# Performance work log

Hardware: AMD Instinct MI355X
Metric: run time of the kernel (lower is better)

The kernel has to match this reference:

```python
import jax, jax.numpy as jnp
import numpy as np


def _diag_gather(x):
    # out[b,c,h,w] = x[b,c,h,(h+w)%W]; then transpose last two dims and flatten
    B, C, H, W = x.shape
    idx = (jnp.arange(H)[:, None] + jnp.arange(W)[None, :]) % W
    g = jnp.take_along_axis(x, idx[None, None], axis=3)  # [B,C,H,W]
    return g.transpose(0, 1, 3, 2).reshape(B, C, H * W)


def _antidiag_gather(x):
    B, C, H, W = x.shape
    idx = (jnp.arange(W)[None, :] - jnp.arange(H)[:, None]) % W
    g = jnp.take_along_axis(x, idx[None, None], axis=3)
    return g.transpose(0, 1, 3, 2).reshape(B, C, H * W)


def _diag_scatter(flat, shape):
    # exact inverse of _diag_gather (per-row circular-shift permutation)
    B, C, H, W = shape
    t = flat.reshape(B, C, W, H).transpose(0, 1, 3, 2)  # [B,C,H,W]
    inv = (jnp.arange(W)[None, :] - jnp.arange(H)[:, None]) % W
    return jnp.take_along_axis(t, inv[None, None], axis=3)


def _antidiag_scatter(flat, shape):
    B, C, H, W = shape
    t = flat.reshape(B, C, W, H).transpose(0, 1, 3, 2)
    inv = (jnp.arange(W)[None, :] + jnp.arange(H)[:, None]) % W
    return jnp.take_along_axis(t, inv[None, None], axis=3)


def cross_scan(x):
    # x: [B,C,H,W] -> xs: [B,8,C,L]; 8 scan directions (row, col, flips, diag, antidiag, flips)
    B, C, H, W = x.shape
    L = H * W
    xf = x.reshape(B, C, L)
    xt = x.transpose(0, 1, 3, 2).reshape(B, C, L)
    xd = _diag_gather(x)
    xa = _antidiag_gather(x)
    return jnp.stack(
        [xf, xt, xf[..., ::-1], xt[..., ::-1], xd, xa, xd[..., ::-1], xa[..., ::-1]],
        axis=1,
    )


def cross_merge(ys):
    # ys: [B,8,D,H,W] -> y: [B,D,L]
    B, K, D, H, W = ys.shape
    L = H * W
    ys = ys.reshape(B, K, D, L)
    a = ys[:, 0:2] + ys[:, 2:4][..., ::-1]
    y = a[:, 0] + a[:, 1].reshape(B, D, W, H).transpose(0, 1, 3, 2).reshape(B, D, L)
    b = ys[:, 4:6] + ys[:, 6:8][..., ::-1]
    y = y + _diag_scatter(b[:, 0], (B, D, H, W)).reshape(B, D, L)
    y = y + _antidiag_scatter(b[:, 1], (B, D, H, W)).reshape(B, D, L)
    return y


def selective_scan(u, delta, A, Bs, Cs, Ds):
    # u, delta: [B,KD,L]; A: [KD,N]; Bs, Cs: [B,K,N,L]; Ds: [KD]
    Bn, KD, L = u.shape
    K = Bs.shape[1]
    Dd = KD // K
    N = A.shape[1]
    dA = jnp.exp(delta[:, :, None, :] * A[None, :, :, None])  # [B,KD,N,L]
    Bexp = jnp.broadcast_to(Bs[:, :, None], (Bn, K, Dd, N, L)).reshape(Bn, KD, N, L)
    Cexp = jnp.broadcast_to(Cs[:, :, None], (Bn, K, Dd, N, L)).reshape(Bn, KD, N, L)
    dBu = delta[:, :, None, :] * Bexp * u[:, :, None, :]

    def comb(c1, c2):
        a1, b1 = c1
        a2, b2 = c2
        return a2 * a1, a2 * b1 + b2

    _, h = jax.lax.associative_scan(comb, (dA, dBu), axis=-1)  # h: [B,KD,N,L]
    return jnp.sum(Cexp * h, axis=2) + Ds[None, :, None] * u


def setup_inputs() -> dict:
    key = jax.random.key(0)
    ks = jax.random.split(key, 8)
    B, D, H, W = 1, 96, 64, 64
    K, N, R = 8, 16, 6
    return {
        "x": jax.random.normal(ks[0], (B, D, H, W), jnp.float32),
        "x_proj_weight": jax.random.normal(ks[1], (K, R + 2 * N, D), jnp.float32) * 0.05,
        "dt_projs_weight": jax.random.normal(ks[2], (K, D, R), jnp.float32) * 0.1,
        "dt_projs_bias": jax.random.normal(ks[3], (K, D), jnp.float32) * 0.1,
        "A_logs": jax.random.uniform(ks[4], (K * D, N), jnp.float32),
        "Ds": jax.random.normal(ks[5], (K * D,), jnp.float32),
        "out_norm_weight": jnp.ones((D,), jnp.float32),
        "out_norm_bias": jnp.zeros((D,), jnp.float32),
    }


def reference(x, x_proj_weight, dt_projs_weight, dt_projs_bias, A_logs, Ds,
              out_norm_weight, out_norm_bias):
    B, D, H, W = x.shape
    K, _, R = dt_projs_weight.shape
    N = A_logs.shape[1]
    L = H * W

    xs = cross_scan(x)  # [B,K,D,L]
    x_dbl = jnp.einsum("bkdl,kcd->bkcl", xs, x_proj_weight)  # [B,K,R+2N,L]
    dts, Bs, Cs = jnp.split(x_dbl, [R, R + N], axis=2)
    dts = jnp.einsum("bkrl,kdr->bkdl", dts, dt_projs_weight)  # [B,K,D,L]

    u = xs.reshape(B, K * D, L)
    delta = jax.nn.softplus(dts.reshape(B, K * D, L)
                            + dt_projs_bias.reshape(-1)[None, :, None])
    A = -jnp.exp(A_logs)  # [KD,N]

    ys = selective_scan(u, delta, A, Bs, Cs, Ds)  # [B,KD,L]
    y = cross_merge(ys.reshape(B, K, D, H, W))  # [B,D,L]

    # out_norm (v0): LayerNorm over channel dim
    y = y.transpose(0, 2, 1)  # [B,L,D]
    mu = jnp.mean(y, axis=-1, keepdims=True)
    var = jnp.var(y, axis=-1, keepdims=True)
    y = (y - mu) * jax.lax.rsqrt(var + 1e-5) * out_norm_weight + out_norm_bias
    return y.reshape(B, H, W, D)
```

## Files before the change

kernel.cpp:

```cpp
#include <hip/hip_runtime.h>
#include <math.h>

#define D_ 96
#define L_ 4096
#define K_ 8
#define N_ 16
#define R_ 6
#define CDBL 38
#define DL_ (D_ * L_)

#define REPN(M) M(0) M(1) M(2) M(3) M(4) M(5) M(6) M(7) \
                M(8) M(9) M(10) M(11) M(12) M(13) M(14) M(15)
#define REP8(M) M(0) M(1) M(2) M(3) M(4) M(5) M(6) M(7)
#define FENCE asm volatile("" ::: "memory");

#if __has_builtin(__builtin_amdgcn_exp2f)
#define EXP2(x) __builtin_amdgcn_exp2f(x)
#else
#define EXP2(x) exp2f(x)
#endif
#if __has_builtin(__builtin_amdgcn_logf)
#define LOG2F(x) __builtin_amdgcn_logf(x)
#else
#define LOG2F(x) __log2f(x)
#endif

#define LOG2E 1.44269504088896340736f
#define LN2F  0.69314718055994530942f

__device__ __forceinline__ int src_index(int k, int l) {
    int h = l & 63, w = l >> 6;
    int lp = 4095 - l;
    int hp = lp & 63, wp = lp >> 6;
    switch (k) {
    case 0: return l;
    case 1: return (h << 6) + w;
    case 2: return lp;
    case 3: return (hp << 6) + wp;
    case 4: return (h << 6) + ((h + w) & 63);
    case 5: return (h << 6) + ((w - h) & 63);
    case 6: return (hp << 6) + ((hp + wp) & 63);
    default: return (hp << 6) + ((wp - hp) & 63);
    }
}

__device__ __forceinline__ int merge_src(int k, int l) {
    int h = l >> 6, w = l & 63;
    int i1 = (w << 6) + h;
    int i4 = (((w - h) & 63) << 6) + h;
    int i5 = (((w + h) & 63) << 6) + h;
    switch (k) {
    case 0: return l;
    case 1: return i1;
    case 2: return 4095 - l;
    case 3: return 4095 - i1;
    case 4: return i4;
    case 5: return i5;
    case 6: return 4095 - i4;
    default: return 4095 - i5;
    }
}

#define PQ(p) ((((p) >> 6) * 66) + ((p) & 63))

__global__ __launch_bounds__(512) void k_xscan(const float* __restrict__ x,
                                               float* __restrict__ xs) {
    __shared__ float img[64 * 66];
    int d = blockIdx.x;
    int t = threadIdx.x;
    const float* xd = x + d * L_;
    #pragma unroll
    for (int i = 0; i < 8; ++i) {
        int l = i * 512 + t;
        img[PQ(l)] = xd[l];
    }
    __syncthreads();
    #pragma unroll
    for (int k = 0; k < K_; ++k) {
        float* dst = xs + (k * D_ + d) * L_;
        #pragma unroll
        for (int i = 0; i < 8; ++i) {
            int l = i * 512 + t;
            dst[l] = img[PQ(src_index(k, l))];
        }
    }
}

__global__ __launch_bounds__(256) void k_xdbl(const float* __restrict__ xs,
                                              const float* __restrict__ wproj,
                                              float* __restrict__ xdbl) {
    __shared__ float tile[64][100];
    int bid = blockIdx.x;
    int swz = (bid & 7) * 64 + (bid >> 3);
    int k = swz >> 6;
    int l0 = (swz & 63) * 64;

    const float* src = xs + k * DL_ + l0;
    for (int e = threadIdx.x; e < D_ * 64; e += 256) {
        int d = e >> 6, li = e & 63;
        tile[li][d] = src[d * L_ + li];
    }
    __syncthreads();

    int lt = threadIdx.x & 63;
    int cg = __builtin_amdgcn_readfirstlane(threadIdx.x >> 6);
    const float* wk = wproj + k * CDBL * D_;
    float acc[10];
    #pragma unroll
    for (int j = 0; j < 10; ++j) acc[j] = 0.f;
    for (int d4 = 0; d4 < D_; d4 += 4) {
        float4 tv = *(const float4*)&tile[lt][d4];
        #pragma unroll
        for (int j = 0; j < 10; ++j) {
            int c = cg + 4 * j;
            if (c < CDBL) {
                float4 wv = *(const float4*)&wk[c * D_ + d4];
                acc[j] = fmaf(tv.x, wv.x, acc[j]);
                acc[j] = fmaf(tv.y, wv.y, acc[j]);
                acc[j] = fmaf(tv.z, wv.z, acc[j]);
                acc[j] = fmaf(tv.w, wv.w, acc[j]);
            }
        }
    }
    #pragma unroll
    for (int j = 0; j < 10; ++j) {
        int c = cg + 4 * j;
        if (c < CDBL) xdbl[(k * CDBL + c) * L_ + l0 + lt] = acc[j];
    }
}


#if __has_builtin(__builtin_amdgcn_update_dpp)
#define HAVE_DPP 1
template<int CTRL, int RM>
__device__ __forceinline__ float updpp(float oldv, float src) {
    int r = __builtin_amdgcn_update_dpp(__builtin_bit_cast(int, oldv),
                                        __builtin_bit_cast(int, src),
                                        CTRL, RM, 0xF, false);
    return __builtin_bit_cast(float, r);
}
#else
#define HAVE_DPP 0
#endif

__global__ __launch_bounds__(512, 3) void k_scan(const float* __restrict__ xdbl,
                                                 const float* __restrict__ dtw,
                                                 const float* __restrict__ dtb,
                                                 const float* __restrict__ alogs,
                                                 const float* __restrict__ dsv_,
                                                 const float* __restrict__ xs,
                                                 float* __restrict__ ys) {
    int bid = blockIdx.x;
    int k = bid & 7;
    int d = bid >> 3;
    int kd = k * D_ + d;
    int t = threadIdx.x;
    int lane = t & 63, wv = t >> 6;
    int l0t = t * 8;

    __shared__ float An_s[16];
    __shared__ float agg_a[8][16], agg_b[8][16];
    __shared__ float cb_s[8][16];
    if (t < 16)
        An_s[t] = -expf(alogs[kd * N_ + t]);

#define DECL(n) float sA##n, sB##n;
    REPN(DECL)
#undef DECL
#define DECL(i) float d##i, u##i, y##i;
    REP8(DECL)
#undef DECL

    const float* xr = xdbl + k * CDBL * L_;
    const float2* wp2 = (const float2*)(dtw + kd * R_);
    const float2 w01 = wp2[0], w23 = wp2[1], w45 = wp2[2];
    const float bias = dtb[kd];
    const float dval = dsv_[kd];
#define SPL2(dst, s) { float p = (s) * LOG2E; \
    float l2 = LOG2F(1.f + EXP2(p)); \
    dst = ((s) > 20.f) ? p : l2; }
#define DLTQ(j, i0, i1, i2, i3) { \
    const float4 r0 = *(const float4*)(xr + 0 * L_ + l0t + j * 4); \
    const float4 r1 = *(const float4*)(xr + 1 * L_ + l0t + j * 4); \
    const float4 r2 = *(const float4*)(xr + 2 * L_ + l0t + j * 4); \
    const float4 r3 = *(const float4*)(xr + 3 * L_ + l0t + j * 4); \
    const float4 r4 = *(const float4*)(xr + 4 * L_ + l0t + j * 4); \
    const float4 r5 = *(const float4*)(xr + 5 * L_ + l0t + j * 4); \
    float s; \
    s = fmaf(w01.x, r0.x, bias); s = fmaf(w01.y, r1.x, s); s = fmaf(w23.x, r2.x, s); \
    s = fmaf(w23.y, r3.x, s); s = fmaf(w45.x, r4.x, s); s = fmaf(w45.y, r5.x, s); \
    SPL2(d##i0, s) \
    s = fmaf(w01.x, r0.y, bias); s = fmaf(w01.y, r1.y, s); s = fmaf(w23.x, r2.y, s); \
    s = fmaf(w23.y, r3.y, s); s = fmaf(w45.x, r4.y, s); s = fmaf(w45.y, r5.y, s); \
    SPL2(d##i1, s) \
    s = fmaf(w01.x, r0.z, bias); s = fmaf(w01.y, r1.z, s); s = fmaf(w23.x, r2.z, s); \
    s = fmaf(w23.y, r3.z, s); s = fmaf(w45.x, r4.z, s); s = fmaf(w45.y, r5.z, s); \
    SPL2(d##i2, s) \
    s = fmaf(w01.x, r0.w, bias); s = fmaf(w01.y, r1.w, s); s = fmaf(w23.x, r2.w, s); \
    s = fmaf(w23.y, r3.w, s); s = fmaf(w45.x, r4.w, s); s = fmaf(w45.y, r5.w, s); \
    SPL2(d##i3, s) }
    DLTQ(0, 0, 1, 2, 3)
    DLTQ(1, 4, 5, 6, 7)
#undef DLTQ
#undef SPL2

    {
        const float* up = xs + kd * L_ + l0t;
        const float4 ua = *(const float4*)(up);
        const float4 ub = *(const float4*)(up + 4);
        u0 = ua.x; u1 = ua.y; u2 = ua.z; u3 = ua.w;
        u4 = ub.x; u5 = ub.y; u6 = ub.z; u7 = ub.w;
    }
#define UG(i) y##i = dval * u##i; u##i *= LN2F; u##i *= d##i;
    REP8(UG)
#undef UG

    __syncthreads();

    const float* Bptr = xdbl + (k * CDBL + R_) * L_ + l0t;
    const float* Cptr = Bptr + N_ * L_;

#define PHA_E(i, Bc) { float e = EXP2(d##i * An); \
    rb = fmaf(e, rb, u##i * (Bc)); ra *= e; }
#define PHA(n) { \
    const float An = An_s[n]; \
    const float* Bn = Bptr + n * L_; \
    const float4 b0 = *(const float4*)(Bn), b1 = *(const float4*)(Bn + 4); \
    float ra = 1.f, rb = 0.f; \
    PHA_E(0, b0.x) PHA_E(1, b0.y) PHA_E(2, b0.z) PHA_E(3, b0.w) \
    PHA_E(4, b1.x) PHA_E(5, b1.y) PHA_E(6, b1.z) PHA_E(7, b1.w) \
    sA##n = ra; sB##n = rb; }
    PHA(0) PHA(1) PHA(2) PHA(3) FENCE
    PHA(4) PHA(5) PHA(6) PHA(7) FENCE
    PHA(8) PHA(9) PHA(10) PHA(11) FENCE
    PHA(12) PHA(13) PHA(14) PHA(15) FENCE
#undef PHA
#undef PHA_E

#if HAVE_DPP
#define SSTN(n) { float pa = updpp<SC_CTRL, SC_RM>(1.f, sA##n); \
                  float pb = updpp<SC_CTRL, SC_RM>(0.f, sB##n); \
                  sB##n = fmaf(sA##n, pb, sB##n); sA##n *= pa; }
#define SC_CTRL 0x111
#define SC_RM 0xF
    REPN(SSTN)
#undef SC_CTRL
#undef SC_RM
#define SC_CTRL 0x112
#define SC_RM 0xF
    REPN(SSTN)
#undef SC_CTRL
#undef SC_RM
#define SC_CTRL 0x114
#define SC_RM 0xF
    REPN(SSTN)
#undef SC_CTRL
#undef SC_RM
#define SC_CTRL 0x118
#define SC_RM 0xF
    REPN(SSTN)
#undef SC_CTRL
#undef SC_RM
#define SC_CTRL 0x142
#define SC_RM 0xA
    REPN(SSTN)
#undef SC_CTRL
#undef SC_RM
#define SC_CTRL 0x143
#define SC_RM 0xC
    REPN(SSTN)
#undef SC_CTRL
#undef SC_RM
#undef SSTN

#define PPREF(n) { \
    if (lane == 63) { agg_a[wv][n] = sA##n; agg_b[wv][n] = sB##n; } \
    sA##n = updpp<0x138, 0xF>(1.f, sA##n); \
    sB##n = updpp<0x138, 0xF>(0.f, sB##n); }
    REPN(PPREF)
#undef PPREF
#else
#define PBF(n) { float pa = __shfl_up(sA##n, off); float pb = __shfl_up(sB##n, off); \
    if (lane >= off) { sB##n = fmaf(sA##n, pb, sB##n); sA##n *= pa; } }
    for (int off = 1; off < 64; off <<= 1) { REPN(PBF) }
#undef PBF
#define PPREF(n) { float ia = sA##n, ib = sB##n; \
    float ea = __shfl_up(ia, 1); float eb = __shfl_up(ib, 1); \
    if (lane == 0) { ea = 1.f; eb = 0.f; } \
    if (lane == 63) { agg_a[wv][n] = ia; agg_b[wv][n] = ib; } \
    sA##n = ea; sB##n = eb; }
    REPN(PPREF)
#undef PPREF
#endif
    __syncthreads();

    if (t < 128) {
        int w = t >> 4, n = t & 15;
        float cb = 0.f;
        for (int w2 = 0; w2 < w; ++w2)
            cb = fmaf(agg_a[w2][n], cb, agg_b[w2][n]);
        cb_s[w][n] = cb;
    }
    __syncthreads();
#define PC(n) { sA##n = fmaf(sA##n, cb_s[wv][n], sB##n); }
    REPN(PC)
#undef PC

#define PHD_E(i, Bc, Cc) { float e = EXP2(d##i * An); \
    h = fmaf(e, h, u##i * (Bc)); y##i = fmaf((Cc), h, y##i); }
#define PHD(n) { \
    const float An = An_s[n]; float h = sA##n; \
    const float* Bn = Bptr + n * L_; const float* Cn = Cptr + n * L_; \
    const float4 b0 = *(const float4*)(Bn), b1 = *(const float4*)(Bn + 4); \
    const float4 c0 = *(const float4*)(Cn), c1 = *(const float4*)(Cn + 4); \
    PHD_E(0, b0.x, c0.x) PHD_E(1, b0.y, c0.y) PHD_E(2, b0.z, c0.z) PHD_E(3, b0.w, c0.w) \
    PHD_E(4, b1.x, c1.x) PHD_E(5, b1.y, c1.y) PHD_E(6, b1.z, c1.z) PHD_E(7, b1.w, c1.w) }
    PHD(0) PHD(1) FENCE
    PHD(2) PHD(3) FENCE
    PHD(4) PHD(5) FENCE
    PHD(6) PHD(7) FENCE
    PHD(8) PHD(9) FENCE
    PHD(10) PHD(11) FENCE
    PHD(12) PHD(13) FENCE
    PHD(14) PHD(15) FENCE
#undef PHD
#undef PHD_E

    float* yp = ys + kd * L_ + l0t;
    {
        float4 o;
        o.x = y0; o.y = y1; o.z = y2; o.w = y3; *(float4*)(yp + 0) = o;
        o.x = y4; o.y = y5; o.z = y6; o.w = y7; *(float4*)(yp + 4) = o;
    }
}

__global__ __launch_bounds__(512) void k_merge(const float* __restrict__ ys,
                                               float* __restrict__ ym) {
    __shared__ float buf[64 * 66];
    int d = blockIdx.x;
    int t = threadIdx.x;
    float a0 = 0.f, a1 = 0.f, a2 = 0.f, a3 = 0.f,
          a4 = 0.f, a5 = 0.f, a6 = 0.f, a7 = 0.f;
    #pragma unroll
    for (int k = 0; k < K_; ++k) {
        const float* srow = ys + (k * D_ + d) * L_;
        #pragma unroll
        for (int i = 0; i < 8; ++i) {
            int l = i * 512 + t;
            buf[PQ(l)] = srow[l];
        }
        __syncthreads();
#define MACC(i) { int l = i * 512 + t; a##i += buf[PQ(merge_src(k, l))]; }
        REP8(MACC)
#undef MACC
        __syncthreads();
    }
    float* drow = ym + d * L_;
#define MST(i) drow[i * 512 + t] = a##i;
    REP8(MST)
#undef MST
}

__global__ __launch_bounds__(512) void k_ln(const float* __restrict__ ym,
                                            const float* __restrict__ gamma,
                                            const float* __restrict__ beta,
                                            float* __restrict__ out) {
    __shared__ float tile[D_ * 65];
    __shared__ float pS[8][64], pQ[8][64];
    __shared__ float mu_s[64], rs_s[64];
    int t = threadIdx.x;
    int lb = blockIdx.x * 64;

    #pragma unroll
    for (int i = 0; i < 12; ++i) {
        int e = i * 512 + t;
        int dd = e >> 6, l_loc = e & 63;
        tile[dd * 65 + l_loc] = ym[dd * L_ + lb + l_loc];
    }
    __syncthreads();

    {
        int wgrp = t >> 6, l_loc = t & 63;
        float s = 0.f, sq = 0.f;
        #pragma unroll
        for (int j = 0; j < 12; ++j) {
            float v = tile[(wgrp * 12 + j) * 65 + l_loc];
            s += v; sq = fmaf(v, v, sq);
        }
        pS[wgrp][l_loc] = s; pQ[wgrp][l_loc] = sq;
    }
    __syncthreads();
    if (t < 64) {
        float s = 0.f, sq = 0.f;
        #pragma unroll
        for (int w2 = 0; w2 < 8; ++w2) { s += pS[w2][t]; sq += pQ[w2][t]; }
        float mu = s * (1.f / 96.f);
        float var = sq * (1.f / 96.f) - mu * mu;
        mu_s[t] = mu;
        rs_s[t] = rsqrtf(var + 1e-5f);
    }
    __syncthreads();

    #pragma unroll
    for (int i = 0; i < 12; ++i) {
        int e = i * 512 + t;
        int l_loc = e / 96, dd = e - l_loc * 96;
        float v = tile[dd * 65 + l_loc];
        float o = fmaf((v - mu_s[l_loc]) * rs_s[l_loc], gamma[dd], beta[dd]);
        out[lb * 96 + e] = o;
    }
}

extern "C" void kernel_launch(void* const* d_in, const int* in_sizes, int n_in,
                              void* d_out, int out_size, void* d_ws, size_t ws_size,
                              hipStream_t stream) {
    const float* x     = (const float*)d_in[0];
    const float* wproj = (const float*)d_in[1];
    const float* dtw   = (const float*)d_in[2];
    const float* dtb   = (const float*)d_in[3];
    const float* alogs = (const float*)d_in[4];
    const float* dsv   = (const float*)d_in[5];
    const float* gamma = (const float*)d_in[6];
    const float* beta  = (const float*)d_in[7];
    float* out = (float*)d_out;
    float* ws  = (float*)d_ws;

    float* xs   = ws;
    float* xdbl = ws + 3145728;
    float* ym   = ws + 4390912;

    hipLaunchKernelGGL(k_xscan, dim3(96), dim3(512), 0, stream, x, xs);
    hipLaunchKernelGGL(k_xdbl, dim3(512), dim3(256), 0, stream, xs, wproj, xdbl);
    hipLaunchKernelGGL(k_scan, dim3(768), dim3(512), 0, stream,
                       xdbl, dtw, dtb, alogs, dsv, xs, xs );
    hipLaunchKernelGGL(k_merge, dim3(96), dim3(512), 0, stream, xs, ym);
    hipLaunchKernelGGL(k_ln, dim3(64), dim3(512), 0, stream, ym, gamma, beta, out);
}
```

Measured before the change: 89.02 us.

## Widen grids across xscan, merge, LN and halve scan block size

Several kernels are re-partitioned to launch more blocks. k_xscan now runs one block per (direction, channel) instead of per channel. k_merge splits the eight directions into two halves that write partial sums, and k_ln adds the halves and works on 16-position tiles with 256 threads. k_scan moves to 256 threads with 16 elements per thread, which lengthens each thread's serial chain and raises register pressure in exchange for fewer cross-wave steps. The aim is better CU occupancy on the small-grid kernels, at the cost of extra workspace traffic for the partial merge buffers and redundant image loads in xscan.

```diff
diff --git a/kernel.cpp b/kernel.cpp
--- a/kernel.cpp
+++ b/kernel.cpp
@@ -63,26 +63,25 @@
 
 #define PQ(p) ((((p) >> 6) * 66) + ((p) & 63))
 
-__global__ __launch_bounds__(512) void k_xscan(const float* __restrict__ x,
+__global__ __launch_bounds__(256) void k_xscan(const float* __restrict__ x,
                                                float* __restrict__ xs) {
     __shared__ float img[64 * 66];
-    int d = blockIdx.x;
+    int bid = blockIdx.x;
+    int k = bid & 7;
+    int d = bid >> 3;
     int t = threadIdx.x;
     const float* xd = x + d * L_;
     #pragma unroll
-    for (int i = 0; i < 8; ++i) {
-        int l = i * 512 + t;
+    for (int i = 0; i < 16; ++i) {
+        int l = i * 256 + t;
         img[PQ(l)] = xd[l];
     }
     __syncthreads();
-    #pragma unroll
-    for (int k = 0; k < K_; ++k) {
-        float* dst = xs + (k * D_ + d) * L_;
-        #pragma unroll
-        for (int i = 0; i < 8; ++i) {
-            int l = i * 512 + t;
-            dst[l] = img[PQ(src_index(k, l))];
-        }
+    float* dst = xs + (k * D_ + d) * L_;
+    #pragma unroll
+    for (int i = 0; i < 16; ++i) {
+        int l = i * 256 + t;
+        dst[l] = img[PQ(src_index(k, l))];
     }
 }
 
@@ -143,7 +142,7 @@
 #define HAVE_DPP 0
 #endif
 
-__global__ __launch_bounds__(512, 3) void k_scan(const float* __restrict__ xdbl,
+__global__ __launch_bounds__(256, 4) void k_scan(const float* __restrict__ xdbl,
                                                  const float* __restrict__ dtw,
                                                  const float* __restrict__ dtb,
                                                  const float* __restrict__ alogs,
@@ -156,11 +155,11 @@
     int kd = k * D_ + d;
     int t = threadIdx.x;
     int lane = t & 63, wv = t >> 6;
-    int l0t = t * 8;
+    int l0t = t * 16;
 
     __shared__ float An_s[16];
-    __shared__ float agg_a[8][16], agg_b[8][16];
-    __shared__ float cb_s[8][16];
+    __shared__ float agg_a[4][16], agg_b[4][16];
+    __shared__ float cb_s[4][16];
     if (t < 16)
         An_s[t] = -expf(alogs[kd * N_ + t]);
 
@@ -168,7 +167,7 @@
     REPN(DECL)
 #undef DECL
 #define DECL(i) float d##i, u##i, y##i;
-    REP8(DECL)
+    REPN(DECL)
 #undef DECL
 
     const float* xr = xdbl + k * CDBL * L_;
@@ -199,8 +198,10 @@
     s = fmaf(w01.x, r0.w, bias); s = fmaf(w01.y, r1.w, s); s = fmaf(w23.x, r2.w, s); \
     s = fmaf(w23.y, r3.w, s); s = fmaf(w45.x, r4.w, s); s = fmaf(w45.y, r5.w, s); \
     SPL2(d##i3, s) }
-    DLTQ(0, 0, 1, 2, 3)
-    DLTQ(1, 4, 5, 6, 7)
+    DLTQ(0, 0, 1, 2, 3)   FENCE
+    DLTQ(1, 4, 5, 6, 7)   FENCE
+    DLTQ(2, 8, 9, 10, 11) FENCE
+    DLTQ(3, 12, 13, 14, 15)
 #undef DLTQ
 #undef SPL2
 
@@ -208,11 +209,15 @@
         const float* up = xs + kd * L_ + l0t;
         const float4 ua = *(const float4*)(up);
         const float4 ub = *(const float4*)(up + 4);
+        const float4 uc = *(const float4*)(up + 8);
+        const float4 ud = *(const float4*)(up + 12);
         u0 = ua.x; u1 = ua.y; u2 = ua.z; u3 = ua.w;
         u4 = ub.x; u5 = ub.y; u6 = ub.z; u7 = ub.w;
+        u8 = uc.x; u9 = uc.y; u10 = uc.z; u11 = uc.w;
+        u12 = ud.x; u13 = ud.y; u14 = ud.z; u15 = ud.w;
     }
 #define UG(i) y##i = dval * u##i; u##i *= LN2F; u##i *= d##i;
-    REP8(UG)
+    REPN(UG)
 #undef UG
 
     __syncthreads();
@@ -226,14 +231,15 @@
     const float An = An_s[n]; \
     const float* Bn = Bptr + n * L_; \
     const float4 b0 = *(const float4*)(Bn), b1 = *(const float4*)(Bn + 4); \
+    const float4 b2 = *(const float4*)(Bn + 8), b3 = *(const float4*)(Bn + 12); \
     float ra = 1.f, rb = 0.f; \
     PHA_E(0, b0.x) PHA_E(1, b0.y) PHA_E(2, b0.z) PHA_E(3, b0.w) \
     PHA_E(4, b1.x) PHA_E(5, b1.y) PHA_E(6, b1.z) PHA_E(7, b1.w) \
-    sA##n = ra; sB##n = rb; }
-    PHA(0) PHA(1) PHA(2) PHA(3) FENCE
-    PHA(4) PHA(5) PHA(6) PHA(7) FENCE
-    PHA(8) PHA(9) PHA(10) PHA(11) FENCE
-    PHA(12) PHA(13) PHA(14) PHA(15) FENCE
+    PHA_E(8, b2.x) PHA_E(9, b2.y) PHA_E(10, b2.z) PHA_E(11, b2.w) \
+    PHA_E(12, b3.x) PHA_E(13, b3.y) PHA_E(14, b3.z) PHA_E(15, b3.w) \
+    sA##n = ra; sB##n = rb; \
+    FENCE }
+    REPN(PHA)
 #undef PHA
 #undef PHA_E
 
@@ -294,7 +300,7 @@
 #endif
     __syncthreads();
 
-    if (t < 128) {
+    if (t < 64) {
         int w = t >> 4, n = t & 15;
         float cb = 0.f;
         for (int w2 = 0; w2 < w; ++w2)
@@ -312,37 +318,40 @@
     const float An = An_s[n]; float h = sA##n; \
     const float* Bn = Bptr + n * L_; const float* Cn = Cptr + n * L_; \
     const float4 b0 = *(const float4*)(Bn), b1 = *(const float4*)(Bn + 4); \
+    const float4 b2 = *(const float4*)(Bn + 8), b3 = *(const float4*)(Bn + 12); \
     const float4 c0 = *(const float4*)(Cn), c1 = *(const float4*)(Cn + 4); \
+    const float4 c2 = *(const float4*)(Cn + 8), c3 = *(const float4*)(Cn + 12); \
     PHD_E(0, b0.x, c0.x) PHD_E(1, b0.y, c0.y) PHD_E(2, b0.z, c0.z) PHD_E(3, b0.w, c0.w) \
-    PHD_E(4, b1.x, c1.x) PHD_E(5, b1.y, c1.y) PHD_E(6, b1.z, c1.z) PHD_E(7, b1.w, c1.w) }
-    PHD(0) PHD(1) FENCE
-    PHD(2) PHD(3) FENCE
-    PHD(4) PHD(5) FENCE
-    PHD(6) PHD(7) FENCE
-    PHD(8) PHD(9) FENCE
-    PHD(10) PHD(11) FENCE
-    PHD(12) PHD(13) FENCE
-    PHD(14) PHD(15) FENCE
+    PHD_E(4, b1.x, c1.x) PHD_E(5, b1.y, c1.y) PHD_E(6, b1.z, c1.z) PHD_E(7, b1.w, c1.w) \
+    PHD_E(8, b2.x, c2.x) PHD_E(9, b2.y, c2.y) PHD_E(10, b2.z, c2.z) PHD_E(11, b2.w, c2.w) \
+    PHD_E(12, b3.x, c3.x) PHD_E(13, b3.y, c3.y) PHD_E(14, b3.z, c3.z) PHD_E(15, b3.w, c3.w) \
+    FENCE }
+    REPN(PHD)
 #undef PHD
 #undef PHD_E
 
     float* yp = ys + kd * L_ + l0t;
     {
         float4 o;
-        o.x = y0; o.y = y1; o.z = y2; o.w = y3; *(float4*)(yp + 0) = o;
-        o.x = y4; o.y = y5; o.z = y6; o.w = y7; *(float4*)(yp + 4) = o;
+        o.x = y0;  o.y = y1;  o.z = y2;  o.w = y3;  *(float4*)(yp + 0)  = o;
+        o.x = y4;  o.y = y5;  o.z = y6;  o.w = y7;  *(float4*)(yp + 4)  = o;
+        o.x = y8;  o.y = y9;  o.z = y10; o.w = y11; *(float4*)(yp + 8)  = o;
+        o.x = y12; o.y = y13; o.z = y14; o.w = y15; *(float4*)(yp + 12) = o;
     }
 }
 
 __global__ __launch_bounds__(512) void k_merge(const float* __restrict__ ys,
-                                               float* __restrict__ ym) {
+                                               float* __restrict__ ym2) {
     __shared__ float buf[64 * 66];
-    int d = blockIdx.x;
+    int bid = blockIdx.x;
+    int kg = bid & 1;
+    int d = bid >> 1;
     int t = threadIdx.x;
     float a0 = 0.f, a1 = 0.f, a2 = 0.f, a3 = 0.f,
           a4 = 0.f, a5 = 0.f, a6 = 0.f, a7 = 0.f;
     #pragma unroll
-    for (int k = 0; k < K_; ++k) {
+    for (int kk = 0; kk < 4; ++kk) {
+        int k = kg * 4 + kk;
         const float* srow = ys + (k * D_ + d) * L_;
         #pragma unroll
         for (int i = 0; i < 8; ++i) {
@@ -355,58 +364,57 @@
 #undef MACC
         __syncthreads();
     }
-    float* drow = ym + d * L_;
+    float* drow = ym2 + (kg * D_ + d) * L_;
 #define MST(i) drow[i * 512 + t] = a##i;
     REP8(MST)
 #undef MST
 }
 
-__global__ __launch_bounds__(512) void k_ln(const float* __restrict__ ym,
+__global__ __launch_bounds__(256) void k_ln(const float* __restrict__ ym2,
                                             const float* __restrict__ gamma,
                                             const float* __restrict__ beta,
                                             float* __restrict__ out) {
-    __shared__ float tile[D_ * 65];
-    __shared__ float pS[8][64], pQ[8][64];
-    __shared__ float mu_s[64], rs_s[64];
+    __shared__ float tile[D_][17];
+    __shared__ float pS[16][17], pQ[16][17];
+    __shared__ float mu_s[16], rs_s[16];
     int t = threadIdx.x;
-    int lb = blockIdx.x * 64;
-
-    #pragma unroll
-    for (int i = 0; i < 12; ++i) {
-        int e = i * 512 + t;
-        int dd = e >> 6, l_loc = e & 63;
-        tile[dd * 65 + l_loc] = ym[dd * L_ + lb + l_loc];
-    }
-    __syncthreads();
-
+    int lb = blockIdx.x * 16;
+
+    #pragma unroll
+    for (int i = 0; i < 6; ++i) {
+        int e = i * 256 + t;
+        int dd = e >> 4, ll = e & 15;
+        float v = ym2[dd * L_ + lb + ll] + ym2[DL_ + dd * L_ + lb + ll];
+        tile[dd][ll] = v;
+    }
+    __syncthreads();
     {
-        int wgrp = t >> 6, l_loc = t & 63;
+        int g = t >> 4, ll = t & 15;
         float s = 0.f, sq = 0.f;
         #pragma unroll
-        for (int j = 0; j < 12; ++j) {
-            float v = tile[(wgrp * 12 + j) * 65 + l_loc];
+        for (int j = 0; j < 6; ++j) {
+            float v = tile[g * 6 + j][ll];
             s += v; sq = fmaf(v, v, sq);
         }
-        pS[wgrp][l_loc] = s; pQ[wgrp][l_loc] = sq;
-    }
-    __syncthreads();
-    if (t < 64) {
+        pS[g][ll] = s; pQ[g][ll] = sq;
+    }
+    __syncthreads();
+    if (t < 16) {
         float s = 0.f, sq = 0.f;
         #pragma unroll
-        for (int w2 = 0; w2 < 8; ++w2) { s += pS[w2][t]; sq += pQ[w2][t]; }
+        for (int g = 0; g < 16; ++g) { s += pS[g][t]; sq += pQ[g][t]; }
         float mu = s * (1.f / 96.f);
         float var = sq * (1.f / 96.f) - mu * mu;
         mu_s[t] = mu;
         rs_s[t] = rsqrtf(var + 1e-5f);
     }
     __syncthreads();
-
-    #pragma unroll
-    for (int i = 0; i < 12; ++i) {
-        int e = i * 512 + t;
-        int l_loc = e / 96, dd = e - l_loc * 96;
-        float v = tile[dd * 65 + l_loc];
-        float o = fmaf((v - mu_s[l_loc]) * rs_s[l_loc], gamma[dd], beta[dd]);
+    #pragma unroll
+    for (int i = 0; i < 6; ++i) {
+        int e = i * 256 + t;
+        int ll = e / 96, dd = e - ll * 96;
+        float v = tile[dd][ll];
+        float o = fmaf((v - mu_s[ll]) * rs_s[ll], gamma[dd], beta[dd]);
         out[lb * 96 + e] = o;
     }
 }
@@ -427,12 +435,12 @@
 
     float* xs   = ws;
     float* xdbl = ws + 3145728;
-    float* ym   = ws + 4390912;
-
-    hipLaunchKernelGGL(k_xscan, dim3(96), dim3(512), 0, stream, x, xs);
+    float* ym2  = ws + 4390912;
+
+    hipLaunchKernelGGL(k_xscan, dim3(768), dim3(256), 0, stream, x, xs);
     hipLaunchKernelGGL(k_xdbl, dim3(512), dim3(256), 0, stream, xs, wproj, xdbl);
-    hipLaunchKernelGGL(k_scan, dim3(768), dim3(512), 0, stream,
+    hipLaunchKernelGGL(k_scan, dim3(768), dim3(256), 0, stream,
                        xdbl, dtw, dtb, alogs, dsv, xs, xs );
-    hipLaunchKernelGGL(k_merge, dim3(96), dim3(512), 0, stream, xs, ym);
-    hipLaunchKernelGGL(k_ln, dim3(64), dim3(512), 0, stream, ym, gamma, beta, out);
-}
+    hipLaunchKernelGGL(k_merge, dim3(192), dim3(512), 0, stream, xs, ym2);
+    hipLaunchKernelGGL(k_ln, dim3(256), dim3(256), 0, stream, ym2, gamma, beta, out);
+}
```

Result: slower. 103.6 us (+16.4%).
